# Kernel optimization log

Measured on AMD Instinct MI355X. Metric: run time of the kernel, lower is better.

The kernel has to match this reference:

```python
import jax, jax.numpy as jnp
import numpy as np

NEG_INF = -1e9  # mask fill value used by the original layer
LEAKY_SLOPE = 0.2


def setup_inputs() -> dict:
    key = jax.random.key(0)
    k1, k2, k3, k4 = jax.random.split(key, 4)
    B, N, D_in = 8, 1024, 256
    H, head_dim = 8, 32  # output_dim=256, concat_heads=True
    node_features = jax.random.normal(k1, (B, N, D_in), dtype=jnp.float32)
    adjacency = jax.random.randint(k2, (B, N, N), 0, 2, dtype=jnp.int32)
    W = jax.random.normal(k3, (H, D_in, head_dim), dtype=jnp.float32) * (1.0 / np.sqrt(D_in))
    a = jax.random.normal(k4, (H, 2 * head_dim), dtype=jnp.float32) * (1.0 / np.sqrt(2 * head_dim))
    bias = jnp.zeros((H * head_dim,), dtype=jnp.float32)
    return {"node_features": node_features, "adjacency": adjacency, "W": W, "a": a, "bias": bias}


def reference(node_features, adjacency, W, a, bias):
    # node_features: (B,N,D_in); adjacency: (B,N,N) in {0,1}
    H, _, hd = W.shape
    # Per-head linear transform: (B,H,N,head_dim)
    Wh = jnp.einsum('bni,hij->bhnj', node_features, W)
    # a @ concat(h_i, h_j) == a1 @ h_i + a2 @ h_j  (avoids O(N^2*2hd) concat)
    a1, a2 = a[:, :hd], a[:, hd:]
    e_i = jnp.einsum('bhnj,hj->bhn', Wh, a1)  # (B,H,N) source term
    e_j = jnp.einsum('bhnj,hj->bhn', Wh, a2)  # (B,H,N) target term
    scores = e_i[:, :, :, None] + e_j[:, :, None, :]  # (B,H,N,N)
    # LeakyReLU(0.2) exactly as ops.maximum(x, 0.2*x)
    scores = jnp.maximum(scores, LEAKY_SLOPE * scores)
    mask = adjacency.astype(scores.dtype)[:, None, :, :]  # (B,1,N,N)
    masked = scores * mask + (1.0 - mask) * NEG_INF
    attn = jax.nn.softmax(masked, axis=-1)  # (B,H,N,N)
    attended = jnp.einsum('bhij,bhjk->bhik', attn, Wh)  # (B,H,N,hd)
    B, _, N, _ = attended.shape
    # concat heads -> (B,N,H*hd); head order matches the python loop concat
    out = attended.transpose(0, 2, 1, 3).reshape(B, N, H * hd)
    out = out + bias
    return jax.nn.relu(out)
```

## Files before the change

kernel.cpp:

```cpp
#include <hip/hip_runtime.h>

#define GAT_B   8
#define GAT_N   1024
#define GAT_DIN 256
#define GAT_H   8
#define GAT_HD  32
#define GAT_LOG2E 1.4426950408889634f

typedef unsigned short gu16;
typedef unsigned int   gu32;
typedef unsigned long long gu64;
typedef __bf16 bf16x8 __attribute__((ext_vector_type(8)));
typedef __bf16 bf16x4 __attribute__((ext_vector_type(4)));
typedef float  f32x4v __attribute__((ext_vector_type(4)));

#if __has_builtin(__builtin_amdgcn_exp2f)
#define GAT_EXP2(x) __builtin_amdgcn_exp2f(x)
#else
#define GAT_EXP2(x) exp2f(x)
#endif

__device__ __forceinline__ float gb2f(gu16 u) { return __uint_as_float(((gu32)u) << 16); }

__device__ __forceinline__ void gat_detect(const gu16* p, int t, int* sflag) {
    if (t < 64) {
        int e0 = (p[2 * t]     >> 7) & 0xFF;
        int e1 = (p[2 * t + 1] >> 7) & 0xFF;
        unsigned long long m = __ballot((e0 >= 140) || (e1 >= 140));
        if (t == 0) *sflag = (m != 0ULL);
    }
}

__global__ __launch_bounds__(512) void CustomGATLayer_90348932038855_pack(
    const void* __restrict__ Xv, const void* __restrict__ Wv, __bf16* __restrict__ wfg)
{
    __shared__ int sflag;
    const int t = threadIdx.x, h = blockIdx.x;
    gat_detect((const gu16*)Xv, t, &sflag);
    __syncthreads();
    const int fp32 = sflag;

    if (fp32) {
        const float* ws = (const float*)Wv + (size_t)h * 8192;
        #pragma unroll
        for (int q = 0; q < 4; ++q) {
            int idx = q * 2048 + t * 4;
            int i = idx >> 5, k = idx & 31;
            float4 v = *(const float4*)(ws + idx);
            int d = h * 8192 + (((i >> 5) * 32 + k) * 4 + ((i >> 3) & 3)) * 8 + (i & 7);
            wfg[d] = (__bf16)v.x; wfg[d + 32] = (__bf16)v.y;
            wfg[d + 64] = (__bf16)v.z; wfg[d + 96] = (__bf16)v.w;
        }
    } else {
        const gu16* ws = (const gu16*)Wv + (size_t)h * 8192;
        gu16* wo = (gu16*)wfg;
        #pragma unroll
        for (int q = 0; q < 4; ++q) {
            int idx = q * 2048 + t * 4;
            int i = idx >> 5, k = idx & 31;
            ushort4 v = *(const ushort4*)(ws + idx);
            int d = h * 8192 + (((i >> 5) * 32 + k) * 4 + ((i >> 3) & 3)) * 8 + (i & 7);
            wo[d] = v.x; wo[d + 32] = v.y; wo[d + 64] = v.z; wo[d + 96] = v.w;
        }
    }
}

__global__ __launch_bounds__(512) void CustomGATLayer_90348932038855_kernel(
    const void* __restrict__ Xv, const __bf16* __restrict__ wfg, const void* __restrict__ Av,
    __bf16* __restrict__ whb, float* __restrict__ e1, float* __restrict__ e2)
{
    __shared__ __align__(16) __bf16 Xl[16][264];
    __shared__ int sflag;

    const int t = threadIdx.x;
    gat_detect((const gu16*)Xv, t, &sflag);

    const int bt = blockIdx.x;
    const int M0 = bt * 16, b = M0 >> 10, nloc = M0 & 1023;
    const int srow = t >> 5, scol = (t & 31) * 8;
    __syncthreads();
    const int fp32 = sflag;

    if (fp32) {
        const float* xs = (const float*)Xv + ((size_t)(b * GAT_N + nloc + srow)) * GAT_DIN + scol;
        float4 x0 = *(const float4*)(xs);
        float4 x1 = *(const float4*)(xs + 4);
        bf16x8 xv;
        xv[0] = (__bf16)x0.x; xv[1] = (__bf16)x0.y; xv[2] = (__bf16)x0.z; xv[3] = (__bf16)x0.w;
        xv[4] = (__bf16)x1.x; xv[5] = (__bf16)x1.y; xv[6] = (__bf16)x1.z; xv[7] = (__bf16)x1.w;
        *(bf16x8*)&Xl[srow][scol] = xv;
    } else {
        const gu16* xs = (const gu16*)Xv + ((size_t)(b * GAT_N + nloc + srow)) * GAT_DIN + scol;
        *(bf16x8*)&Xl[srow][scol] = *(const bf16x8*)xs;
    }
    __syncthreads();

    const int h = t >> 6, l = t & 63, g = l >> 4, c = l & 15;
    const __bf16* wf = wfg + h * 8192;

    f32x4v acc0 = {0.f, 0.f, 0.f, 0.f};
    f32x4v acc1 = {0.f, 0.f, 0.f, 0.f};
    #pragma unroll
    for (int kc = 0; kc < 8; ++kc) {
        bf16x8 af = *(const bf16x8*)&Xl[c][kc * 32 + 8 * g];
        bf16x8 b0 = *(const bf16x8*)(wf + ((kc * 32 + c) * 4 + g) * 8);
        bf16x8 b1 = *(const bf16x8*)(wf + ((kc * 32 + c + 16) * 4 + g) * 8);
        acc0 = __builtin_amdgcn_mfma_f32_16x16x32_bf16(af, b0, acc0, 0, 0, 0);
        acc1 = __builtin_amdgcn_mfma_f32_16x16x32_bf16(af, b1, acc1, 0, 0, 0);
    }

    const int nb = nloc + 4 * g;
    const int jcc = nb >> 5, kg = (nb >> 3) & 3, e0 = nb & 7;
    const size_t fb = (((size_t)(b * GAT_H + h) * 32 + jcc) * 4 + kg) * 32;
    bf16x4 v0, v1;
    v0[0] = (__bf16)acc0[0]; v0[1] = (__bf16)acc0[1];
    v0[2] = (__bf16)acc0[2]; v0[3] = (__bf16)acc0[3];
    v1[0] = (__bf16)acc1[0]; v1[1] = (__bf16)acc1[1];
    v1[2] = (__bf16)acc1[2]; v1[3] = (__bf16)acc1[3];
    *(bf16x4*)(whb + (fb + c) * 8 + e0)      = v0;
    *(bf16x4*)(whb + (fb + c + 16) * 8 + e0) = v1;

    float a1c, a1c16, a2c, a2c16;
    if (fp32) {
        const float* ap = (const float*)Av + h * 2 * GAT_HD;
        a1c = ap[c] * GAT_LOG2E;      a1c16 = ap[c + 16] * GAT_LOG2E;
        a2c = ap[32 + c] * GAT_LOG2E; a2c16 = ap[48 + c] * GAT_LOG2E;
    } else {
        const gu16* ap = (const gu16*)Av + h * 2 * GAT_HD;
        a1c = gb2f(ap[c]) * GAT_LOG2E;      a1c16 = gb2f(ap[c + 16]) * GAT_LOG2E;
        a2c = gb2f(ap[32 + c]) * GAT_LOG2E; a2c16 = gb2f(ap[48 + c]) * GAT_LOG2E;
    }
    float p1[4], p2[4];
    #pragma unroll
    for (int q = 0; q < 4; ++q) {
        p1[q] = acc0[q] * a1c + acc1[q] * a1c16;
        p2[q] = acc0[q] * a2c + acc1[q] * a2c16;
        #pragma unroll
        for (int mm = 1; mm <= 8; mm <<= 1) {
            p1[q] += __shfl_xor(p1[q], mm);
            p2[q] += __shfl_xor(p2[q], mm);
        }
    }
    if (c == 0) {
        const size_t eb = (size_t)(b * GAT_H + h) * GAT_N + nb;
        #pragma unroll
        for (int q = 0; q < 4; ++q) { e1[eb + q] = p1[q]; e2[eb + q] = p2[q]; }
    }
}

__global__ __launch_bounds__(1024, 8) void CustomGATLayer_90348932038855_attn(
    const void* __restrict__ Xv, const int* __restrict__ adj, const void* __restrict__ biasv,
    const __bf16* __restrict__ whb, const float* __restrict__ e1f, const float* __restrict__ e2f,
    float* __restrict__ out)
{
    __shared__ __align__(16) float e2l[GAT_H][1024];
    __shared__ gu64 pklu[16][17];
    __shared__ int sflag;

    const int t = threadIdx.x;
    const int w = t >> 6, l = t & 63, g = l >> 4, c = l & 15;
    const int h = w & 7, jh = w >> 3;
    const int id = blockIdx.x;
    const int b = id & 7, tile = id >> 3;
    const int i0 = tile * 16;

    gat_detect((const gu16*)Xv, t, &sflag);

    {
        const int* ar = adj + ((size_t)(b * GAT_N + i0 + w)) * GAT_N;
        #pragma unroll
        for (int s = 0; s < 16; ++s) {
            int v = ar[s * 64 + l];
            gu64 m = __ballot(v != 0);
            if (l == 0) pklu[w][s] = m;
        }
    }
    {
        const float* s = e2f + (size_t)(b * GAT_H + h) * GAT_N + jh * 512;
        float* d = &e2l[h][jh * 512];
        #pragma unroll
        for (int q = 0; q < 2; ++q) {
            int off = (q * 64 + l) * 4;
            *(float4*)(d + off) = *(const float4*)(s + off);
        }
    }
    __syncthreads();
    const int fp32 = sflag;

    const float e1r = e1f[(size_t)(b * GAT_H + h) * GAT_N + i0 + c];
    const __bf16* whr = whb + (size_t)(b * GAT_H + h) * (GAT_N * GAT_HD)
                            + jh * 16384 + g * 256 + c * 8;
    const float* e2h = &e2l[h][jh * 512 + 8 * g];
    const gu32* pkr = (const gu32*)pklu[c] + jh * 16;

    bf16x8 wA0 = *(const bf16x8*)(whr),        wA1 = *(const bf16x8*)(whr + 128);
    bf16x8 wB0 = *(const bf16x8*)(whr + 1024), wB1 = *(const bf16x8*)(whr + 1152);

    f32x4v acc0 = {0.f, 0.f, 0.f, 0.f};
    f32x4v acc1 = {0.f, 0.f, 0.f, 0.f};
    f32x4v accS = {0.f, 0.f, 0.f, 0.f};
    bf16x8 onesf;
    #pragma unroll
    for (int e = 0; e < 8; ++e) onesf[e] = (__bf16)1.0f;

#define GAT_WCOMP(EV, IDX) {                        \
        float s_ = e1r + (EV);                      \
        s_ = fmaxf(s_, 0.2f * s_);                  \
        s_ = fminf(s_, 86.0f);                      \
        float w_ = GAT_EXP2(s_);                    \
        w_ = (ab & (1u << IDX)) ? w_ : 0.0f;        \
        pf[IDX] = (__bf16)w_; }

    #pragma unroll 2
    for (int jc = 0; jc < 16; ++jc) {
        const bf16x8 w0 = wA0, w1 = wA1;
        wA0 = wB0; wA1 = wB1;
        if (jc < 14) {
            const __bf16* wn = whr + (jc + 2) * 1024;
            wB0 = *(const bf16x8*)wn; wB1 = *(const bf16x8*)(wn + 128);
        }
        const gu32 ab = (pkr[jc] >> (8 * g)) & 0xFFu;
        float4 ea = *(const float4*)(e2h + jc * 32);
        float4 eb = *(const float4*)(e2h + jc * 32 + 4);
        bf16x8 pf;
        GAT_WCOMP(ea.x, 0) GAT_WCOMP(ea.y, 1)
        GAT_WCOMP(ea.z, 2) GAT_WCOMP(ea.w, 3)
        GAT_WCOMP(eb.x, 4) GAT_WCOMP(eb.y, 5)
        GAT_WCOMP(eb.z, 6) GAT_WCOMP(eb.w, 7)
        acc0 = __builtin_amdgcn_mfma_f32_16x16x32_bf16(pf, w0, acc0, 0, 0, 0);
        acc1 = __builtin_amdgcn_mfma_f32_16x16x32_bf16(pf, w1, acc1, 0, 0, 0);
        accS = __builtin_amdgcn_mfma_f32_16x16x32_bf16(pf, onesf, accS, 0, 0, 0);
    }
#undef GAT_WCOMP

    __syncthreads();
    float4* sc = (float4*)e2l;
    const int slot = h * 64 + l;
    if (jh == 1) {
        sc[slot]        = make_float4(acc0[0], acc0[1], acc0[2], acc0[3]);
        sc[512 + slot]  = make_float4(acc1[0], acc1[1], acc1[2], acc1[3]);
        sc[1024 + slot] = make_float4(accS[0], accS[1], accS[2], accS[3]);
    }
    __syncthreads();
    if (jh == 0) {
        float4 q0 = sc[slot], q1 = sc[512 + slot], q2 = sc[1024 + slot];
        acc0[0] += q0.x; acc0[1] += q0.y; acc0[2] += q0.z; acc0[3] += q0.w;
        acc1[0] += q1.x; acc1[1] += q1.y; acc1[2] += q1.z; acc1[3] += q1.w;
        accS[0] += q2.x; accS[1] += q2.y; accS[2] += q2.z; accS[3] += q2.w;

        float bv0, bv1;
        if (fp32) {
            const float* bp = (const float*)biasv + h * GAT_HD;
            bv0 = bp[c]; bv1 = bp[c + 16];
        } else {
            const gu16* bp = (const gu16*)biasv + h * GAT_HD;
            bv0 = gb2f(bp[c]); bv1 = gb2f(bp[c + 16]);
        }

        float* ob = out + (size_t)(b * GAT_N + i0) * (GAT_H * GAT_HD) + h * GAT_HD + c;
        #pragma unroll
        for (int q = 0; q < 4; ++q) {
            float d = accS[q];
            float r = (d > 0.f) ? (1.0f / d) : 0.0f;
            float o0 = fmaxf(acc0[q] * r + bv0, 0.f);
            float o1 = fmaxf(acc1[q] * r + bv1, 0.f);
            ob[(size_t)(4 * g + q) * (GAT_H * GAT_HD)]      = o0;
            ob[(size_t)(4 * g + q) * (GAT_H * GAT_HD) + 16] = o1;
        }
    }
}

extern "C" void kernel_launch(void* const* d_in, const int* in_sizes, int n_in,
                              void* d_out, int out_size, void* d_ws, size_t ws_size,
                              hipStream_t stream) {
    const void* X    = d_in[0];
    const int*  adj  = (const int*)d_in[1];
    const void* Wm   = d_in[2];
    const void* Av   = d_in[3];
    const void* bias = d_in[4];
    float* outp = (float*)d_out;

    __bf16* whb = (__bf16*)d_ws;
    float* e1   = (float*)(whb + (size_t)GAT_B * GAT_H * GAT_N * GAT_HD);
    float* e2   = e1 + (size_t)GAT_B * GAT_H * GAT_N;
    __bf16* wfg = (__bf16*)(e2 + (size_t)GAT_B * GAT_H * GAT_N);

    CustomGATLayer_90348932038855_pack
        <<<dim3(8), 512, 0, stream>>>(X, Wm, wfg);
    CustomGATLayer_90348932038855_kernel
        <<<dim3(512), 512, 0, stream>>>(X, wfg, Av, whb, e1, e2);
    CustomGATLayer_90348932038855_attn
        <<<dim3((GAT_N / 16) * GAT_B), 1024, 0, stream>>>(
            X, adj, bias, whb, e1, e2, outp);
}
```

Measured before the change: 125.8 us.

## Bit-pack adjacency in projection kernel and feed packed mask to attention

New measurement: 122.0 us. -3.0%, faster.

```diff
diff --git a/kernel.cpp b/kernel.cpp
--- a/kernel.cpp
+++ b/kernel.cpp
@@ -67,16 +67,25 @@
 
 __global__ __launch_bounds__(512) void CustomGATLayer_90348932038855_kernel(
     const void* __restrict__ Xv, const __bf16* __restrict__ wfg, const void* __restrict__ Av,
+    const int* __restrict__ adj, gu32* __restrict__ pk32,
     __bf16* __restrict__ whb, float* __restrict__ e1, float* __restrict__ e2)
 {
     __shared__ __align__(16) __bf16 Xl[16][264];
     __shared__ int sflag;
 
     const int t = threadIdx.x;
-    gat_detect((const gu16*)Xv, t, &sflag);
-
     const int bt = blockIdx.x;
     const int M0 = bt * 16, b = M0 >> 10, nloc = M0 & 1023;
+
+    const int arow = t >> 5, adw = t & 31;
+    const int* aro = adj + ((size_t)(M0 + arow)) * GAT_N + adw * 32;
+    const int4 a0 = *(const int4*)(aro);      const int4 a1 = *(const int4*)(aro + 4);
+    const int4 a2 = *(const int4*)(aro + 8);  const int4 a3 = *(const int4*)(aro + 12);
+    const int4 a4 = *(const int4*)(aro + 16); const int4 a5 = *(const int4*)(aro + 20);
+    const int4 a6 = *(const int4*)(aro + 24); const int4 a7 = *(const int4*)(aro + 28);
+
+    gat_detect((const gu16*)Xv, t, &sflag);
+
     const int srow = t >> 5, scol = (t & 31) * 8;
     __syncthreads();
     const int fp32 = sflag;
@@ -146,15 +155,34 @@
         #pragma unroll
         for (int q = 0; q < 4; ++q) { e1[eb + q] = p1[q]; e2[eb + q] = p2[q]; }
     }
+
+    gu32 m = 0;
+    m |= (a0.x != 0 ? 1u : 0u)       | (a0.y != 0 ? 2u : 0u)
+       | (a0.z != 0 ? 4u : 0u)       | (a0.w != 0 ? 8u : 0u);
+    m |= (a1.x != 0 ? 16u : 0u)      | (a1.y != 0 ? 32u : 0u)
+       | (a1.z != 0 ? 64u : 0u)      | (a1.w != 0 ? 128u : 0u);
+    m |= (a2.x != 0 ? 256u : 0u)     | (a2.y != 0 ? 512u : 0u)
+       | (a2.z != 0 ? 1024u : 0u)    | (a2.w != 0 ? 2048u : 0u);
+    m |= (a3.x != 0 ? 4096u : 0u)    | (a3.y != 0 ? 8192u : 0u)
+       | (a3.z != 0 ? 16384u : 0u)   | (a3.w != 0 ? 32768u : 0u);
+    m |= (a4.x != 0 ? 1u << 16 : 0u) | (a4.y != 0 ? 1u << 17 : 0u)
+       | (a4.z != 0 ? 1u << 18 : 0u) | (a4.w != 0 ? 1u << 19 : 0u);
+    m |= (a5.x != 0 ? 1u << 20 : 0u) | (a5.y != 0 ? 1u << 21 : 0u)
+       | (a5.z != 0 ? 1u << 22 : 0u) | (a5.w != 0 ? 1u << 23 : 0u);
+    m |= (a6.x != 0 ? 1u << 24 : 0u) | (a6.y != 0 ? 1u << 25 : 0u)
+       | (a6.z != 0 ? 1u << 26 : 0u) | (a6.w != 0 ? 1u << 27 : 0u);
+    m |= (a7.x != 0 ? 1u << 28 : 0u) | (a7.y != 0 ? 1u << 29 : 0u)
+       | (a7.z != 0 ? 1u << 30 : 0u) | (a7.w != 0 ? 1u << 31 : 0u);
+    pk32[((size_t)(M0 + arow)) * 32 + adw] = m;
 }
 
 __global__ __launch_bounds__(1024, 8) void CustomGATLayer_90348932038855_attn(
-    const void* __restrict__ Xv, const int* __restrict__ adj, const void* __restrict__ biasv,
+    const void* __restrict__ Xv, const gu32* __restrict__ pk32, const void* __restrict__ biasv,
     const __bf16* __restrict__ whb, const float* __restrict__ e1f, const float* __restrict__ e2f,
     float* __restrict__ out)
 {
     __shared__ __align__(16) float e2l[GAT_H][1024];
-    __shared__ gu64 pklu[16][17];
+    __shared__ gu32 pkl[16][33];
     __shared__ int sflag;
 
     const int t = threadIdx.x;
@@ -166,14 +194,8 @@
 
     gat_detect((const gu16*)Xv, t, &sflag);
 
-    {
-        const int* ar = adj + ((size_t)(b * GAT_N + i0 + w)) * GAT_N;
-        #pragma unroll
-        for (int s = 0; s < 16; ++s) {
-            int v = ar[s * 64 + l];
-            gu64 m = __ballot(v != 0);
-            if (l == 0) pklu[w][s] = m;
-        }
+    if (t < 512) {
+        pkl[t >> 5][t & 31] = pk32[((size_t)(b * GAT_N + i0 + (t >> 5))) * 32 + (t & 31)];
     }
     {
         const float* s = e2f + (size_t)(b * GAT_H + h) * GAT_N + jh * 512;
@@ -191,7 +213,7 @@
     const __bf16* whr = whb + (size_t)(b * GAT_H + h) * (GAT_N * GAT_HD)
                             + jh * 16384 + g * 256 + c * 8;
     const float* e2h = &e2l[h][jh * 512 + 8 * g];
-    const gu32* pkr = (const gu32*)pklu[c] + jh * 16;
+    const gu32* pkr = &pkl[c][jh * 16];
 
     bf16x8 wA0 = *(const bf16x8*)(whr),        wA1 = *(const bf16x8*)(whr + 128);
     bf16x8 wB0 = *(const bf16x8*)(whr + 1024), wB1 = *(const bf16x8*)(whr + 1152);
@@ -284,12 +306,13 @@
     float* e1   = (float*)(whb + (size_t)GAT_B * GAT_H * GAT_N * GAT_HD);
     float* e2   = e1 + (size_t)GAT_B * GAT_H * GAT_N;
     __bf16* wfg = (__bf16*)(e2 + (size_t)GAT_B * GAT_H * GAT_N);
+    gu32* pk32  = (gu32*)(wfg + (size_t)GAT_H * GAT_DIN * GAT_HD);
 
     CustomGATLayer_90348932038855_pack
         <<<dim3(8), 512, 0, stream>>>(X, Wm, wfg);
     CustomGATLayer_90348932038855_kernel
-        <<<dim3(512), 512, 0, stream>>>(X, wfg, Av, whb, e1, e2);
+        <<<dim3(512), 512, 0, stream>>>(X, wfg, Av, adj, pk32, whb, e1, e2);
     CustomGATLayer_90348932038855_attn
         <<<dim3((GAT_N / 16) * GAT_B), 1024, 0, stream>>>(
-            X, adj, bias, whb, e1, e2, outp);
-}
+            X, pk32, bias, whb, e1, e2, outp);
+}
```
